# Kernel tuning notes

Hardware: AMD Instinct MI355X
Metric: run time of the kernel (lower is better)

Reference implementation:

```python
import jax, jax.numpy as jnp
import numpy as np

B, N, PS = 8, 2048, 32
P = N // PS          # 64 patches
D, MLP, DEPTH, H, DH = 1024, 2048, 6, 8, 64
INNER = H * DH       # 512
K = 20
EPS = 1e-5


def setup_inputs() -> dict:
    key = jax.random.key(0)
    ks = jax.random.split(key, 16)
    r = lambda i, shape: jax.random.normal(ks[i], shape, dtype=jnp.float32) * 0.02
    return {
        "x": jax.random.normal(ks[0], (B, N, 3), dtype=jnp.float32),
        "x_pos_embed": r(1, (B, P + 1, D)),
        "w1": r(2, (64, 6)),   "g1": jnp.ones(64),  "b1": jnp.zeros(64),
        "w2": r(3, (64, 128)), "g2": jnp.ones(64),  "b2": jnp.zeros(64),
        "w3": r(4, (128, 128)),"g3": jnp.ones(128), "b3": jnp.zeros(128),
        "w4": r(5, (256, 256)),"g4": jnp.ones(256), "b4": jnp.zeros(256),
        "w5": r(6, (D, 512)),  "g5": jnp.ones(D),   "b5": jnp.zeros(D),
        "cls_token": r(7, (1, 1, D)),
        "ln1_g": jnp.ones((DEPTH, D)), "ln1_b": jnp.zeros((DEPTH, D)),
        "wqkv": r(8, (DEPTH, D, 3 * INNER)),
        "wout": r(9, (DEPTH, INNER, D)), "bout": jnp.zeros((DEPTH, D)),
        "ln2_g": jnp.ones((DEPTH, D)), "ln2_b": jnp.zeros((DEPTH, D)),
        "wff1": r(10, (DEPTH, D, MLP)), "bff1": jnp.zeros((DEPTH, MLP)),
        "wff2": r(11, (DEPTH, MLP, D)), "bff2": jnp.zeros((DEPTH, D)),
    }


def _knn(x, k):  # x: [B, C, N] -> neighbor idx [B, N, k]
    xx = jnp.sum(x * x, axis=1)                        # [B, N]
    inner = jnp.einsum('bcn,bcm->bnm', x, x)           # [B, N, N]
    dist = 2.0 * inner - xx[:, :, None] - xx[:, None, :]  # = -||xi-xj||^2
    return jax.lax.top_k(dist, k)[1]


def _graph_feature(x, k):  # x: [B, C, N] -> [B, N, k, 2C]
    idx = _knn(x, k)
    xt = jnp.transpose(x, (0, 2, 1))                   # [B, N, C]
    nbr = jax.vmap(lambda f, i: f[i])(xt, idx)         # gather: [B, N, k, C]
    ctr = jnp.broadcast_to(xt[:, :, None, :], nbr.shape)
    return jnp.concatenate([nbr - ctr, ctr], axis=-1)


def _leaky(v):
    return jnp.where(v >= 0, v, 0.2 * v)


def _edge_conv(x, w, g, b, k):  # EdgeConv block: graph feat -> 1x1 conv -> BN(train) -> lrelu -> max over k
    f = _graph_feature(x, k)                           # [B, N, k, 2C]
    y = jnp.einsum('bnkc,oc->bonk', f, w)              # [B, O, N, k]
    mu = jnp.mean(y, axis=(0, 2, 3), keepdims=True)
    var = jnp.var(y, axis=(0, 2, 3), keepdims=True)
    y = (y - mu) * jax.lax.rsqrt(var + EPS) * g[None, :, None, None] + b[None, :, None, None]
    return jnp.max(_leaky(y), axis=-1)                 # [B, O, N]


def _ln(x, g, b):
    mu = jnp.mean(x, axis=-1, keepdims=True)
    var = jnp.var(x, axis=-1, keepdims=True)
    return (x - mu) * jax.lax.rsqrt(var + EPS) * g + b


def reference(x, x_pos_embed, w1, g1, b1, w2, g2, b2, w3, g3, b3, w4, g4, b4,
              w5, g5, b5, cls_token, ln1_g, ln1_b, wqkv, wout, bout,
              ln2_g, ln2_b, wff1, bff1, wff2, bff2):
    scale = DH ** -0.5
    pts = jnp.transpose(x, (0, 2, 1))                  # [B, 3, N]
    x1 = _edge_conv(pts, w1, g1, b1, K)                # [B, 64, N]
    x2 = _edge_conv(x1, w2, g2, b2, K)                 # [B, 64, N]
    x3 = _edge_conv(x2, w3, g3, b3, K)                 # [B, 128, N]
    x4 = _edge_conv(x3, w4, g4, b4, K)                 # [B, 256, N]
    h = jnp.concatenate([x1, x2, x3, x4], axis=1)      # [B, 512, N]
    y = jnp.einsum('bcn,oc->bon', h, w5)               # conv5 1x1 -> [B, D, N]
    mu = jnp.mean(y, axis=(0, 2), keepdims=True)
    var = jnp.var(y, axis=(0, 2), keepdims=True)
    y = _leaky((y - mu) * jax.lax.rsqrt(var + EPS) * g5[None, :, None] + b5[None, :, None])
    # patch max-pool: 'b (p n) c -> (b p) n c' then max over n
    t = jnp.transpose(y, (0, 2, 1)).reshape(B * P, PS, D)
    t = jnp.max(t, axis=1).reshape(B, P, D)
    t = jnp.concatenate([jnp.broadcast_to(cls_token, (B, 1, D)), t], axis=1)  # [B, P+1, D]
    for i in range(DEPTH):
        t = t + x_pos_embed
        hn = _ln(t, ln1_g[i], ln1_b[i])
        qkv = (hn @ wqkv[i]).reshape(B, P + 1, 3, H, DH)
        q, k_, v = [jnp.transpose(qkv[:, :, j], (0, 2, 1, 3)) for j in range(3)]
        attn = jax.nn.softmax(jnp.einsum('bhld,bhmd->bhlm', q, k_) * scale, axis=-1)
        z = jnp.einsum('bhlm,bhmd->bhld', attn, v)
        z = jnp.transpose(z, (0, 2, 1, 3)).reshape(B, P + 1, INNER)
        t = t + z @ wout[i] + bout[i]
        hn = _ln(t, ln2_g[i], ln2_b[i])
        t = t + jax.nn.gelu(hn @ wff1[i] + bff1[i], approximate=False) @ wff2[i] + bff2[i]
    return t[:, 1:]                                    # [B, P, D]
```

## Files before the change

kernel.cpp:

```cpp
#include <hip/hip_runtime.h>
#include <math.h>

#define BB 8
#define NN 2048
#define PSZ 32
#define PP 64
#define DD 1024
#define MLPD 2048
#define DEPTH_ 6
#define HH 8
#define DHH 64
#define INNER_ 512
#define KK 20
#define TOK 65
#define EPSF 1e-5f

#define GEMM_ACC 1
#define GEMM_GELU 2
#define GEMM_OUTBF16 4

typedef __bf16 bf16_t;
typedef __attribute__((ext_vector_type(8))) __bf16 bf16x8;
typedef __attribute__((ext_vector_type(4))) float f32x4;

__device__ __forceinline__ void async_copy16(const bf16_t* gsrc, bf16_t* ldst) {
    __builtin_amdgcn_global_load_lds(
        (const __attribute__((address_space(1))) unsigned int*)gsrc,
        (__attribute__((address_space(3))) unsigned int*)ldst,
        16, 0, 0);
}

__global__ void transpose_x_kernel(const float* __restrict__ x, float* __restrict__ pts) {
    int gid = blockIdx.x * blockDim.x + threadIdx.x;
    if (gid >= BB * NN * 3) return;
    int c = gid % 3; int n = (gid / 3) % NN; int b = gid / (3 * NN);
    pts[(b * 3 + c) * NN + n] = x[gid];
}

__global__ void sqnorm_kernel(const float* __restrict__ x, int bs, int C, float* __restrict__ xx) {
    int gid = blockIdx.x * blockDim.x + threadIdx.x;
    if (gid >= BB * NN) return;
    int n = gid % NN; int b = gid / NN;
    const float* xp = x + b * bs + n;
    float s = 0.f;
    for (int c = 0; c < C; ++c) { float v = xp[c * NN]; s += v * v; }
    xx[gid] = s;
}

__global__ __launch_bounds__(256) void dist_kernel(const float* __restrict__ x, int bs, int C,
                                                   const float* __restrict__ xx, int b0,
                                                   float* __restrict__ dist) {
    __shared__ __align__(16) float smem[4224];
    float (*As)[132] = (float(*)[132])smem;
    float (*Bs)[132] = (float(*)[132])(smem + 16 * 132);
    float (*tb)[132] = (float(*)[132])smem;

    int q = blockIdx.x;
    int bi = 0, rem = q;
    while (rem >= (16 - bi)) { rem -= (16 - bi); ++bi; }
    int bj = bi + rem;

    int b = b0 + blockIdx.z;
    int n0 = bi * 128, m0 = bj * 128;
    int tid = threadIdx.x;
    int ty = tid >> 4, tx = tid & 15;
    float acc[2][2][4][4] = {};
    const float* xb = x + (long)b * bs;
    for (int k0 = 0; k0 < C; k0 += 16) {
        #pragma unroll
        for (int p = 0; p < 2; ++p) {
            int li = tid + p * 256;
            int i4 = li & 31;
            int kk = li >> 5;
            int c = k0 + kk;
            float4 va = make_float4(0.f, 0.f, 0.f, 0.f);
            float4 vb = va;
            if (c < C) {
                va = *(const float4*)&xb[(long)c * NN + n0 + i4 * 4];
                vb = *(const float4*)&xb[(long)c * NN + m0 + i4 * 4];
            }
            *(float4*)&As[kk][i4 * 4] = va;
            *(float4*)&Bs[kk][i4 * 4] = vb;
        }
        __syncthreads();
        #pragma unroll
        for (int kk = 0; kk < 16; ++kk) {
            float a[2][4], bv[2][4];
            *(float4*)a[0] = *(const float4*)&As[kk][ty * 4];
            *(float4*)a[1] = *(const float4*)&As[kk][64 + ty * 4];
            *(float4*)bv[0] = *(const float4*)&Bs[kk][tx * 4];
            *(float4*)bv[1] = *(const float4*)&Bs[kk][64 + tx * 4];
            #pragma unroll
            for (int ri = 0; ri < 2; ++ri)
                #pragma unroll
                for (int ci = 0; ci < 2; ++ci)
                    #pragma unroll
                    for (int i = 0; i < 4; ++i)
                        #pragma unroll
                        for (int j = 0; j < 4; ++j)
                            acc[ri][ci][i][j] += a[ri][i] * bv[ci][j];
        }
        __syncthreads();
    }
    float* db = dist + (long)blockIdx.z * NN * NN;
    const float* xxb = xx + b * NN;
    float xm[2][4];
    #pragma unroll
    for (int ci = 0; ci < 2; ++ci)
        #pragma unroll
        for (int j = 0; j < 4; ++j)
            xm[ci][j] = xxb[m0 + ci * 64 + tx * 4 + j];
    #pragma unroll
    for (int ri = 0; ri < 2; ++ri)
        #pragma unroll
        for (int i = 0; i < 4; ++i) {
            float xn = xxb[n0 + ri * 64 + ty * 4 + i];
            #pragma unroll
            for (int ci = 0; ci < 2; ++ci)
                #pragma unroll
                for (int j = 0; j < 4; ++j)
                    acc[ri][ci][i][j] = 2.f * acc[ri][ci][i][j] - xn - xm[ci][j];
        }
    #pragma unroll
    for (int ri = 0; ri < 2; ++ri)
        #pragma unroll
        for (int i = 0; i < 4; ++i) {
            int n = n0 + ri * 64 + ty * 4 + i;
            #pragma unroll
            for (int ci = 0; ci < 2; ++ci)
                *(float4*)&db[(long)n * NN + m0 + ci * 64 + tx * 4] = *(float4*)&acc[ri][ci][i][0];
        }
    if (bi != bj) {
        #pragma unroll
        for (int s = 0; s < 4; ++s) {
            __syncthreads();
            int ci = s >> 1;
            if ((tx >> 3) == (s & 1)) {
                #pragma unroll
                for (int ri = 0; ri < 2; ++ri)
                    #pragma unroll
                    for (int j = 0; j < 4; ++j) {
                        float4 v;
                        v.x = acc[ri][ci][0][j];
                        v.y = acc[ri][ci][1][j];
                        v.z = acc[ri][ci][2][j];
                        v.w = acc[ri][ci][3][j];
                        *(float4*)&tb[(tx & 7) * 4 + j][ri * 64 + ty * 4] = v;
                    }
            }
            __syncthreads();
            int r = tid >> 3;
            int c0 = (tid & 7) * 16;
            long orow = (long)(m0 + s * 32 + r) * NN + n0 + c0;
            #pragma unroll
            for (int c4 = 0; c4 < 4; ++c4)
                *(float4*)&db[orow + c4 * 4] = *(const float4*)&tb[r][c0 + c4 * 4];
        }
    }
}

__global__ __launch_bounds__(256) void topk_kernel(const float* __restrict__ dist, int b0,
                                                   int* __restrict__ idx) {
    __shared__ float cval[4][64];
    __shared__ int   cidx[4][64];
    int b = b0 + blockIdx.y;
    int wid = threadIdx.x >> 6, lane = threadIdx.x & 63;
    int n = blockIdx.x * 4 + wid;
    const float* row = dist + ((long)blockIdx.y * NN + n) * NN;
    float vals[32];
    #pragma unroll
    for (int s = 0; s < 32; ++s) vals[s] = row[s * 64 + lane];
    int* op = idx + ((long)b * NN + n) * KK;

    float lm = vals[0];
    #pragma unroll
    for (int s = 1; s < 32; ++s) lm = fmaxf(lm, vals[s]);

    float sv = lm;
    #pragma unroll
    for (int k = 2; k <= 64; k <<= 1) {
        #pragma unroll
        for (int j = k >> 1; j > 0; j >>= 1) {
            float pv = __shfl_xor(sv, j);
            bool lower = (lane & j) == 0;
            bool up = (lane & k) != 0;
            bool ownBetter = sv > pv;
            bool keepOwn = ownBetter ^ (lower == up);
            sv = keepOwn ? sv : pv;
        }
    }
    float t = __shfl(sv, 19);

    int base = 0;
    #pragma unroll
    for (int s = 0; s < 32; ++s) {
        bool q = vals[s] >= t;
        unsigned long long m = __ballot(q);
        int my = base + (int)__builtin_amdgcn_mbcnt_hi((unsigned)(m >> 32),
                         __builtin_amdgcn_mbcnt_lo((unsigned)m, 0u));
        if (q && my < 64) { cval[wid][my] = vals[s]; cidx[wid][my] = s * 64 + lane; }
        base += (int)__popcll(m);
    }
    __asm__ volatile("s_waitcnt lgkmcnt(0)" ::: "memory");

    if (base <= 64) {
        float v = (lane < base) ? cval[wid][lane] : -INFINITY;
        int   ii = (lane < base) ? cidx[wid][lane] : 0x7FFFFFFF;
        #pragma unroll
        for (int k = 2; k <= 64; k <<= 1) {
            #pragma unroll
            for (int j = k >> 1; j > 0; j >>= 1) {
                float pv = __shfl_xor(v, j);
                int   pi = __shfl_xor(ii, j);
                bool lower = (lane & j) == 0;
                bool up = (lane & k) != 0;
                bool ownBetter = (v > pv) || (v == pv && ii < pi);
                bool keepOwn = ownBetter ^ (lower == up);
                if (!keepOwn) { v = pv; ii = pi; }
            }
        }
        if (lane < KK) op[lane] = ii;
    } else {
        for (int kk = 0; kk < KK; ++kk) {
            float bv = vals[0]; int bsl = 0;
            #pragma unroll
            for (int s = 1; s < 32; ++s) if (vals[s] > bv) { bv = vals[s]; bsl = s; }
            int bm = bsl * 64 + lane;
            for (int off = 32; off; off >>= 1) {
                float ov = __shfl_xor(bv, off);
                int om = __shfl_xor(bm, off);
                if (ov > bv || (ov == bv && om < bm)) { bv = ov; bm = om; }
            }
            int wslot = bm >> 6, wlane = bm & 63;
            #pragma unroll
            for (int s = 0; s < 32; ++s)
                if (s == wslot) vals[s] = (lane == wlane) ? -INFINITY : vals[s];
            if (lane == 0) op[kk] = bm;
        }
    }
}

__global__ __launch_bounds__(256) void pq_kernel(const float* __restrict__ x, int bs, int C,
                                                 const float* __restrict__ w, int O,
                                                 float* __restrict__ p, float* __restrict__ q) {
    __shared__ float wT[256][33];
    __shared__ float xs[128][32];
    int b = blockIdx.z;
    int o0 = blockIdx.y * 32;
    int n0 = blockIdx.x * 32;
    int tid = threadIdx.x;
    for (int i = tid; i < 2 * C * 32; i += 256) {
        int c2 = i % (2 * C), o = i / (2 * C);
        wT[c2][o] = w[(o0 + o) * 2 * C + c2];
    }
    for (int i = tid; i < C * 32; i += 256) {
        int nl = i % 32, c = i / 32;
        xs[c][nl] = x[b * bs + c * NN + n0 + nl];
    }
    __syncthreads();
    int o_l = tid & 31;
    int n_base = (tid >> 5) * 4;
    float ps[4] = {0.f, 0.f, 0.f, 0.f};
    float qs[4] = {0.f, 0.f, 0.f, 0.f};
    for (int c = 0; c < C; ++c) {
        float4 xv = *(const float4*)&xs[c][n_base];
        float wa = wT[c][o_l];
        float wb = wT[C + c][o_l];
        float d = wb - wa;
        ps[0] += xv.x * wa; qs[0] += xv.x * d;
        ps[1] += xv.y * wa; qs[1] += xv.y * d;
        ps[2] += xv.z * wa; qs[2] += xv.z * d;
        ps[3] += xv.w * wa; qs[3] += xv.w * d;
    }
    for (int j = 0; j < 4; ++j) {
        long r = (long)(b * NN + n0 + n_base + j) * O + o0 + o_l;
        p[r] = ps[j];
        q[r] = qs[j];
    }
}

__global__ void zero_stats_kernel(double* __restrict__ s1, double* __restrict__ s2) {
    int t = blockIdx.x * blockDim.x + threadIdx.x;
    if (t < 1024) { s1[t] = 0.0; s2[t] = 0.0; }
}

__global__ __launch_bounds__(256) void edge_stats_kernel(const float* __restrict__ p, const float* __restrict__ q,
                                                         const int* __restrict__ idx, int O,
                                                         double* __restrict__ gsum, double* __restrict__ gsumsq) {
    int tid = threadIdx.x;
    int o = tid % O;
    int grp = tid / O;
    int ngrp = 256 / O;
    int rows_per_blk = (BB * NN) / gridDim.x;
    int r0 = blockIdx.x * rows_per_blk;
    double s = 0.0, ss = 0.0;
    for (int r = r0 + grp; r < r0 + rows_per_blk; r += ngrp) {
        int b = r / NN;
        float qv = q[r * O + o];
        for (int k = 0; k < KK; ++k) {
            int j = idx[r * KK + k];
            float v = p[(b * NN + j) * O + o] + qv;
            s += v; ss += (double)v * v;
        }
    }
    atomicAdd(&gsum[o], s);
    atomicAdd(&gsumsq[o], ss);
}

__global__ void bn_finalize_kernel(const double* __restrict__ gsum, const double* __restrict__ gsumsq,
                                   const float* __restrict__ g, const float* __restrict__ bb, int O, double cnt,
                                   float* __restrict__ scale, float* __restrict__ shift) {
    int o = blockIdx.x * blockDim.x + threadIdx.x;
    if (o >= O) return;
    double mean = gsum[o] / cnt;
    double var = gsumsq[o] / cnt - mean * mean;
    float inv = rsqrtf((float)var + EPSF);
    float sc = g[o] * inv;
    scale[o] = sc;
    shift[o] = bb[o] - (float)mean * sc;
}

__global__ void edge_out_kernel(const float* __restrict__ p, const float* __restrict__ q,
                                const int* __restrict__ idx, int O,
                                const float* __restrict__ scale, const float* __restrict__ shift,
                                float* __restrict__ out, int obs) {
    int gid = blockIdx.x * blockDim.x + threadIdx.x;
    if (gid >= BB * NN * O) return;
    int o = gid % O; int n = (gid / O) % NN; int b = gid / (O * NN);
    int r = b * NN + n;
    float qv = q[r * O + o];
    float sc = scale[o], sh = shift[o];
    float m = -INFINITY;
    for (int k = 0; k < KK; ++k) {
        int j = idx[r * KK + k];
        float v = (p[(b * NN + j) * O + o] + qv) * sc + sh;
        v = (v >= 0.f) ? v : 0.2f * v;
        m = fmaxf(m, v);
    }
    out[b * obs + o * NN + n] = m;
}

__global__ __launch_bounds__(256) void transpose_cvt_kernel(const float* __restrict__ in,
                                                            bf16_t* __restrict__ outp,
                                                            int R, int C, long s_in, long s_out) {
    __shared__ float tile[32][33];
    const float* ib = in + (long)blockIdx.z * s_in;
    bf16_t* ob = outp + (long)blockIdx.z * s_out;
    int r0 = blockIdx.y * 32, c0 = blockIdx.x * 32;
    int tx = threadIdx.x & 31, tg = threadIdx.x >> 5;
    for (int i = 0; i < 4; ++i) {
        int r = tg + i * 8;
        tile[r][tx] = ib[(long)(r0 + r) * C + c0 + tx];
    }
    __syncthreads();
    for (int i = 0; i < 4; ++i) {
        int c = tg + i * 8;
        ob[(long)(c0 + c) * R + r0 + tx] = (bf16_t)tile[tx][c];
    }
}

__global__ void cvt_bf16_kernel(const float* __restrict__ in, bf16_t* __restrict__ outp, long n8) {
    long g = (long)blockIdx.x * blockDim.x + threadIdx.x;
    if (g >= n8) return;
    const float4* pp = (const float4*)(in + g * 8);
    float4 a = pp[0], b = pp[1];
    bf16x8 v;
    v[0] = (bf16_t)a.x; v[1] = (bf16_t)a.y; v[2] = (bf16_t)a.z; v[3] = (bf16_t)a.w;
    v[4] = (bf16_t)b.x; v[5] = (bf16_t)b.y; v[6] = (bf16_t)b.z; v[7] = (bf16_t)b.w;
    *(bf16x8*)(outp + g * 8) = v;
}

__global__ __launch_bounds__(256) void gemm_bf16_kernel(const bf16_t* __restrict__ A,
                                                        const bf16_t* __restrict__ Bt,
                                                        const float* __restrict__ bias,
                                                        float* __restrict__ out,
                                                        int M, int Kd, int Nd,
                                                        long sA, long sBt, long sO, int flags) {
    __shared__ __align__(16) bf16_t As[64 * 32];
    __shared__ __align__(16) bf16_t Bs[64 * 32];
    const bf16_t* Ab = A + (long)blockIdx.z * sA;
    const bf16_t* Bb = Bt + (long)blockIdx.z * sBt;
    int row0 = blockIdx.y * 64, col0 = blockIdx.x * 64;
    int tid = threadIdx.x;
    int lane = tid & 63, wv = tid >> 6;
    int wm = wv >> 1, wn = wv & 1;
    int srow = tid & 63;
    int sk = wv * 8;
    const bf16_t* ap = Ab + (long)(row0 + srow) * Kd + sk;
    const bf16_t* bp = Bb + (long)(col0 + srow) * Kd + sk;
    bf16_t* lA = &As[wv * 512];
    bf16_t* lB = &Bs[wv * 512];
    f32x4 acc[2][2] = {};
    for (int k0 = 0; k0 < Kd; k0 += 32) {
        async_copy16(ap + k0, lA);
        async_copy16(bp + k0, lB);
        __syncthreads();
        int q = lane >> 4, cl = lane & 15;
        bf16x8 a0v = *(const bf16x8*)&As[(q * 64 + wm * 32 + cl) * 8];
        bf16x8 a1v = *(const bf16x8*)&As[(q * 64 + wm * 32 + 16 + cl) * 8];
        bf16x8 b0v = *(const bf16x8*)&Bs[(q * 64 + wn * 32 + cl) * 8];
        bf16x8 b1v = *(const bf16x8*)&Bs[(q * 64 + wn * 32 + 16 + cl) * 8];
        acc[0][0] = __builtin_amdgcn_mfma_f32_16x16x32_bf16(a0v, b0v, acc[0][0], 0, 0, 0);
        acc[0][1] = __builtin_amdgcn_mfma_f32_16x16x32_bf16(a0v, b1v, acc[0][1], 0, 0, 0);
        acc[1][0] = __builtin_amdgcn_mfma_f32_16x16x32_bf16(a1v, b0v, acc[1][0], 0, 0, 0);
        acc[1][1] = __builtin_amdgcn_mfma_f32_16x16x32_bf16(a1v, b1v, acc[1][1], 0, 0, 0);
        __syncthreads();
    }
    int q = lane >> 4, cl = lane & 15;
    float* Obf = out + (long)blockIdx.z * sO;
    bf16_t* Obh = (bf16_t*)out + (long)blockIdx.z * sO;
    for (int mt = 0; mt < 2; ++mt)
        for (int nt = 0; nt < 2; ++nt)
            #pragma unroll
            for (int r = 0; r < 4; ++r) {
                int row = row0 + wm * 32 + mt * 16 + q * 4 + r;
                if (row >= M) continue;
                int col = col0 + wn * 32 + nt * 16 + cl;
                float v = acc[mt][nt][r];
                if (bias) v += bias[col];
                if (flags & GEMM_GELU) v = 0.5f * v * (1.f + erff(v * 0.70710678118654752f));
                long oidx = (long)row * Nd + col;
                if (flags & GEMM_OUTBF16) Obh[oidx] = (bf16_t)v;
                else if (flags & GEMM_ACC) Obf[oidx] += v;
                else Obf[oidx] = v;
            }
}

__global__ __launch_bounds__(256) void bn5_stats_bf16_kernel(const bf16_t* __restrict__ y5,
                                                             const float* __restrict__ g,
                                                             const float* __restrict__ bb,
                                                             float* __restrict__ scale, float* __restrict__ shift) {
    __shared__ double ssum[256], ssq[256];
    int d = blockIdx.x;
    int tid = threadIdx.x;
    double s = 0.0, sq = 0.0;
    for (int b = 0; b < BB; ++b) {
        const bf16_t* row = y5 + ((long)b * DD + d) * NN;
        for (int n = tid; n < NN; n += 256) { float v = (float)row[n]; s += v; sq += (double)v * v; }
    }
    ssum[tid] = s; ssq[tid] = sq;
    __syncthreads();
    for (int st = 128; st > 0; st >>= 1) {
        if (tid < st) { ssum[tid] += ssum[tid + st]; ssq[tid] += ssq[tid + st]; }
        __syncthreads();
    }
    if (tid == 0) {
        double cnt = (double)BB * NN;
        double mean = ssum[0] / cnt;
        double var = ssq[0] / cnt - mean * mean;
        float inv = rsqrtf((float)var + EPSF);
        float sc = g[d] * inv;
        scale[d] = sc;
        shift[d] = bb[d] - (float)mean * sc;
    }
}

__global__ void pool_bf16_kernel(const bf16_t* __restrict__ y5, const float* __restrict__ scale,
                                 const float* __restrict__ shift, const float* __restrict__ cls,
                                 float* __restrict__ t) {
    int gid = blockIdx.x * blockDim.x + threadIdx.x;
    if (gid >= BB * TOK * DD) return;
    int d = gid % DD; int l = (gid / DD) % TOK; int b = gid / (DD * TOK);
    float v;
    if (l == 0) {
        v = cls[d];
    } else {
        int pp = l - 1;
        const bf16_t* row = y5 + ((long)b * DD + d) * NN + pp * PSZ;
        float sc = scale[d], sh = shift[d];
        float m = -INFINITY;
        for (int i = 0; i < PSZ; ++i) {
            float u = (float)row[i] * sc + sh;
            u = (u >= 0.f) ? u : 0.2f * u;
            m = fmaxf(m, u);
        }
        v = m;
    }
    t[gid] = v;
}

__global__ __launch_bounds__(256) void ln_kernel(float* __restrict__ t, const float* __restrict__ pos,
                                                 const float* __restrict__ g, const float* __restrict__ bb,
                                                 bf16_t* __restrict__ hn, int addpos) {
    __shared__ double s1[256], s2[256];
    long r = blockIdx.x;
    int tid = threadIdx.x;
    float vals[4];
    double s = 0.0, sq = 0.0;
    for (int i = 0; i < 4; ++i) {
        int d = tid + i * 256;
        float v = t[r * DD + d];
        if (addpos) { v += pos[r * DD + d]; t[r * DD + d] = v; }
        vals[i] = v; s += v; sq += (double)v * v;
    }
    s1[tid] = s; s2[tid] = sq;
    __syncthreads();
    for (int st = 128; st > 0; st >>= 1) {
        if (tid < st) { s1[tid] += s1[tid + st]; s2[tid] += s2[tid + st]; }
        __syncthreads();
    }
    double mean = s1[0] / DD;
    float var = (float)(s2[0] / DD - mean * mean);
    float fm = (float)mean;
    float inv = rsqrtf(var + EPSF);
    for (int i = 0; i < 4; ++i) {
        int d = tid + i * 256;
        hn[r * DD + d] = (bf16_t)((vals[i] - fm) * inv * g[d] + bb[d]);
    }
}

__global__ __launch_bounds__(256) void attn_kernel(const float* __restrict__ qkv, bf16_t* __restrict__ z) {
    __shared__ float ks[TOK][DHH + 1];
    __shared__ float vs[TOK][DHH + 1];
    __shared__ float ss[TOK][TOK];
    int bh = blockIdx.x;
    int b = bh / HH, h = bh % HH;
    int tid = threadIdx.x;
    for (int i = tid; i < TOK * DHH; i += 256) {
        int l = i / DHH, d = i % DHH;
        long base = (long)(b * TOK + l) * 1536;
        ks[l][d] = qkv[base + 512 + h * DHH + d];
        vs[l][d] = qkv[base + 1024 + h * DHH + d];
    }
    __syncthreads();
    for (int i = tid; i < TOK * TOK; i += 256) {
        int l = i / TOK, m = i % TOK;
        const float* qrow = qkv + (long)(b * TOK + l) * 1536 + h * DHH;
        float acc = 0.f;
        for (int d = 0; d < DHH; ++d) acc += qrow[d] * ks[m][d];
        ss[l][m] = acc * 0.125f;
    }
    __syncthreads();
    if (tid < TOK) {
        float mx = -INFINITY;
        for (int m = 0; m < TOK; ++m) mx = fmaxf(mx, ss[tid][m]);
        float sum = 0.f;
        for (int m = 0; m < TOK; ++m) { float e = expf(ss[tid][m] - mx); ss[tid][m] = e; sum += e; }
        float invs = 1.f / sum;
        for (int m = 0; m < TOK; ++m) ss[tid][m] *= invs;
    }
    __syncthreads();
    for (int i = tid; i < TOK * DHH; i += 256) {
        int l = i / DHH, d = i % DHH;
        float acc = 0.f;
        for (int m = 0; m < TOK; ++m) acc += ss[l][m] * vs[m][d];
        z[(long)(b * TOK + l) * INNER_ + h * DHH + d] = (bf16_t)acc;
    }
}

__global__ void final_kernel(const float* __restrict__ t, float* __restrict__ out) {
    int gid = blockIdx.x * blockDim.x + threadIdx.x;
    if (gid >= BB * PP * DD) return;
    int d = gid % DD; int p = (gid / DD) % PP; int b = gid / (DD * PP);
    out[gid] = t[((long)b * TOK + 1 + p) * DD + d];
}

static inline int ceil_div(long a, long b) { return (int)((a + b - 1) / b); }

extern "C" void kernel_launch(void* const* d_in, const int* in_sizes, int n_in,
                              void* d_out, int out_size, void* d_ws, size_t ws_size,
                              hipStream_t stream) {
    const float* x    = (const float*)d_in[0];
    const float* pos  = (const float*)d_in[1];
    const float* w1   = (const float*)d_in[2];
    const float* g1   = (const float*)d_in[3];
    const float* b1   = (const float*)d_in[4];
    const float* w2   = (const float*)d_in[5];
    const float* g2   = (const float*)d_in[6];
    const float* b2   = (const float*)d_in[7];
    const float* w3   = (const float*)d_in[8];
    const float* g3   = (const float*)d_in[9];
    const float* b3   = (const float*)d_in[10];
    const float* w4   = (const float*)d_in[11];
    const float* g4   = (const float*)d_in[12];
    const float* b4   = (const float*)d_in[13];
    const float* w5   = (const float*)d_in[14];
    const float* g5   = (const float*)d_in[15];
    const float* b5   = (const float*)d_in[16];
    const float* cls  = (const float*)d_in[17];
    const float* ln1g = (const float*)d_in[18];
    const float* ln1b = (const float*)d_in[19];
    const float* wqkv = (const float*)d_in[20];
    const float* wout = (const float*)d_in[21];
    const float* bout = (const float*)d_in[22];
    const float* ln2g = (const float*)d_in[23];
    const float* ln2b = (const float*)d_in[24];
    const float* wff1 = (const float*)d_in[25];
    const float* bff1 = (const float*)d_in[26];
    const float* wff2 = (const float*)d_in[27];
    const float* bff2 = (const float*)d_in[28];
    float* out = (float*)d_out;

    char* ws = (char*)d_ws;
    size_t off = 0;
    auto alloc = [&](size_t bytes) -> char* {
        char* ptr = ws + off;
        off = (off + bytes + 255) & ~(size_t)255;
        return ptr;
    };
    float*  h      = (float*)alloc((size_t)BB * 512 * NN * 4);
    float*  t      = (float*)alloc((size_t)BB * TOK * DD * 4);
    bf16_t* hnb    = (bf16_t*)alloc((size_t)BB * TOK * DD * 4);
    float*  qkvb   = (float*)alloc((size_t)BB * TOK * 1536 * 4);
    bf16_t* zbb    = (bf16_t*)alloc((size_t)BB * TOK * INNER_ * 4);
    bf16_t* ubb    = (bf16_t*)alloc((size_t)BB * TOK * MLPD * 4);
    double* dsum   = (double*)alloc(1024 * 8);
    double* dsq    = (double*)alloc(1024 * 8);
    float*  scaleb = (float*)alloc(1024 * 4);
    float*  shiftb = (float*)alloc(1024 * 4);
    size_t ubase = off;

    size_t uoff = ubase;
    auto ualloc = [&](size_t bytes) -> char* {
        char* ptr = ws + uoff;
        uoff = (uoff + bytes + 255) & ~(size_t)255;
        return ptr;
    };
    float* pts  = (float*)ualloc((size_t)BB * 3 * NN * 4);
    float* xx   = (float*)ualloc((size_t)BB * NN * 4);
    int*   idxb = (int*)  ualloc((size_t)BB * NN * KK * 4);
    float* pbuf = (float*)ualloc((size_t)BB * NN * 256 * 4);
    float* qbuf = (float*)ualloc((size_t)BB * NN * 256 * 4);
    size_t dist_rel = uoff - ubase;
    float* distb = (float*)(ws + uoff);

    size_t voff = ubase;
    auto valloc = [&](size_t bytes) -> char* {
        char* ptr = ws + voff;
        voff = (voff + bytes + 255) & ~(size_t)255;
        return ptr;
    };
    bf16_t* hT     = (bf16_t*)valloc((size_t)BB * NN * 512 * 2);
    bf16_t* wTqkv  = (bf16_t*)valloc((size_t)DEPTH_ * 1536 * DD * 2);
    bf16_t* wTout  = (bf16_t*)valloc((size_t)DEPTH_ * DD * INNER_ * 2);
    bf16_t* wTff1  = (bf16_t*)valloc((size_t)DEPTH_ * MLPD * DD * 2);
    bf16_t* wTff2  = (bf16_t*)valloc((size_t)DEPTH_ * DD * MLPD * 2);
    bf16_t* w5b    = (bf16_t*)valloc((size_t)DD * 512 * 2);
    size_t stage_bf16 = voff - ubase;

    size_t conv_full  = dist_rel + (size_t)BB * NN * NN * 4;
    size_t conv_batch = dist_rel + (size_t)NN * NN * 4;

    auto mx = [](size_t a, size_t b) { return a > b ? a : b; };
    bool use_bf16 = ws_size >= ubase + mx(conv_batch, stage_bf16);
    bool full     = ws_size >= ubase + mx(conv_full, stage_bf16);
    if (!use_bf16) return;
    bf16_t* y5bf = (bf16_t*)h;

    transpose_x_kernel<<<ceil_div((long)BB * NN * 3, 256), 256, 0, stream>>>(x, pts);

    const int NTRI = 136;
    auto run_conv = [&](const float* xin, int xbs, int C, const float* w,
                        const float* g, const float* bb, float* hout, int O) {
        sqnorm_kernel<<<ceil_div((long)BB * NN, 256), 256, 0, stream>>>(xin, xbs, C, xx);
        if (full) {
            dist_kernel<<<dim3(NTRI, 1, BB), 256, 0, stream>>>(xin, xbs, C, xx, 0, distb);
            topk_kernel<<<dim3(NN / 4, BB), 256, 0, stream>>>(distb, 0, idxb);
        } else {
            for (int b = 0; b < BB; ++b) {
                dist_kernel<<<dim3(NTRI, 1, 1), 256, 0, stream>>>(xin, xbs, C, xx, b, distb);
                topk_kernel<<<dim3(NN / 4, 1), 256, 0, stream>>>(distb, b, idxb);
            }
        }
        {
            dim3 grid(NN / 32, O / 32, BB);
            pq_kernel<<<grid, 256, 0, stream>>>(xin, xbs, C, w, O, pbuf, qbuf);
        }
        zero_stats_kernel<<<4, 256, 0, stream>>>(dsum, dsq);
        edge_stats_kernel<<<256, 256, 0, stream>>>(pbuf, qbuf, idxb, O, dsum, dsq);
        bn_finalize_kernel<<<1, 256, 0, stream>>>(dsum, dsq, g, bb, O, (double)BB * NN * KK, scaleb, shiftb);
        edge_out_kernel<<<ceil_div((long)BB * NN * O, 256), 256, 0, stream>>>(
            pbuf, qbuf, idxb, O, scaleb, shiftb, hout, 512 * NN);
    };
    run_conv(pts, 3 * NN, 3, w1, g1, b1, h, 64);
    run_conv(h, 512 * NN, 64, w2, g2, b2, h + 64 * NN, 64);
    run_conv(h + 64 * NN, 512 * NN, 64, w3, g3, b3, h + 128 * NN, 128);
    run_conv(h + 128 * NN, 512 * NN, 128, w4, g4, b4, h + 256 * NN, 256);

    const int M = BB * TOK;

    transpose_cvt_kernel<<<dim3(NN / 32, 512 / 32, BB), 256, 0, stream>>>(
        h, hT, 512, NN, (long)512 * NN, (long)NN * 512);
    transpose_cvt_kernel<<<dim3(1536 / 32, DD / 32, DEPTH_), 256, 0, stream>>>(
        wqkv, wTqkv, DD, 1536, (long)DD * 1536, (long)1536 * DD);
    transpose_cvt_kernel<<<dim3(DD / 32, INNER_ / 32, DEPTH_), 256, 0, stream>>>(
        wout, wTout, INNER_, DD, (long)INNER_ * DD, (long)DD * INNER_);
    transpose_cvt_kernel<<<dim3(MLPD / 32, DD / 32, DEPTH_), 256, 0, stream>>>(
        wff1, wTff1, DD, MLPD, (long)DD * MLPD, (long)MLPD * DD);
    transpose_cvt_kernel<<<dim3(DD / 32, MLPD / 32, DEPTH_), 256, 0, stream>>>(
        wff2, wTff2, MLPD, DD, (long)MLPD * DD, (long)DD * MLPD);
    cvt_bf16_kernel<<<ceil_div((long)DD * 512 / 8, 256), 256, 0, stream>>>(w5, w5b, (long)DD * 512 / 8);

    gemm_bf16_kernel<<<dim3(NN / 64, DD / 64, BB), 256, 0, stream>>>(
        w5b, hT, nullptr, (float*)y5bf, DD, 512, NN, 0L, (long)NN * 512, (long)DD * NN, GEMM_OUTBF16);
    bn5_stats_bf16_kernel<<<DD, 256, 0, stream>>>(y5bf, g5, b5, scaleb, shiftb);
    pool_bf16_kernel<<<ceil_div((long)BB * TOK * DD, 256), 256, 0, stream>>>(y5bf, scaleb, shiftb, cls, t);

    for (int i = 0; i < DEPTH_; ++i) {
        ln_kernel<<<M, 256, 0, stream>>>(t, pos, ln1g + i * DD, ln1b + i * DD, hnb, 1);
        gemm_bf16_kernel<<<dim3(1536 / 64, ceil_div(M, 64), 1), 256, 0, stream>>>(
            hnb, wTqkv + (size_t)i * 1536 * DD, nullptr, qkvb, M, DD, 1536, 0L, 0L, 0L, 0);
        attn_kernel<<<BB * HH, 256, 0, stream>>>(qkvb, zbb);
        gemm_bf16_kernel<<<dim3(DD / 64, ceil_div(M, 64), 1), 256, 0, stream>>>(
            zbb, wTout + (size_t)i * DD * INNER_, bout + i * DD, t, M, INNER_, DD, 0L, 0L, 0L, GEMM_ACC);
        ln_kernel<<<M, 256, 0, stream>>>(t, nullptr, ln2g + i * DD, ln2b + i * DD, hnb, 0);
        gemm_bf16_kernel<<<dim3(MLPD / 64, ceil_div(M, 64), 1), 256, 0, stream>>>(
            hnb, wTff1 + (size_t)i * MLPD * DD, bff1 + i * MLPD, (float*)ubb, M, DD, MLPD,
            0L, 0L, 0L, GEMM_GELU | GEMM_OUTBF16);
        gemm_bf16_kernel<<<dim3(DD / 64, ceil_div(M, 64), 1), 256, 0, stream>>>(
            ubb, wTff2 + (size_t)i * DD * MLPD, bff2 + i * DD, t, M, MLPD, DD, 0L, 0L, 0L, GEMM_ACC);
    }

    final_kernel<<<ceil_div((long)BB * PP * DD, 256), 256, 0, stream>>>(t, out);
}
```

Baseline: 2.018 ms.

## Fuse edge-conv stats and max/min gather, finalize via affine monotonicity

Adds a single gather pass that computes the batch-norm sums and also the per-row max and min of the k neighbour values. A small finalize kernel then applies the BN affine and leaky ReLU to the max (or to the min when the scale is negative) and writes the transposed output through a shared-memory tile. This removes the second pass over the k gathered neighbours in edge_out. In exchange it writes and reads max/min buffers that reuse the distance scratch region. The new path is taken only when the full workspace is available.

```diff
diff --git a/kernel.cpp b/kernel.cpp
--- a/kernel.cpp
+++ b/kernel.cpp
@@ -284,6 +284,75 @@
     if (t < 1024) { s1[t] = 0.0; s2[t] = 0.0; }
 }
 
+__global__ __launch_bounds__(256) void edge_gather_kernel(const float* __restrict__ p,
+                                                          const float* __restrict__ q,
+                                                          const int* __restrict__ idx, int O,
+                                                          double* __restrict__ gsum,
+                                                          double* __restrict__ gsumsq,
+                                                          float* __restrict__ maxb,
+                                                          float* __restrict__ minb) {
+    int tid = threadIdx.x;
+    int o = tid % O;
+    int grp = tid / O;
+    int ngrp = 256 / O;
+    int rows_per_blk = (BB * NN) / gridDim.x;
+    int r0 = blockIdx.x * rows_per_blk;
+    double s = 0.0, ss = 0.0;
+    for (int r = r0 + grp; r < r0 + rows_per_blk; r += ngrp) {
+        int b = r / NN;
+        float qv = q[(long)r * O + o];
+        const int* ip = idx + (long)r * KK;
+        float mx = -INFINITY, mn = INFINITY;
+        for (int k = 0; k < KK; ++k) {
+            int j = ip[k];
+            float v = p[(long)(b * NN + j) * O + o] + qv;
+            s += v; ss += (double)v * v;
+            mx = fmaxf(mx, v); mn = fminf(mn, v);
+        }
+        maxb[(long)r * O + o] = mx;
+        minb[(long)r * O + o] = mn;
+    }
+    atomicAdd(&gsum[o], s);
+    atomicAdd(&gsumsq[o], ss);
+}
+
+__global__ void bn_finalize_kernel(const double* __restrict__ gsum, const double* __restrict__ gsumsq,
+                                   const float* __restrict__ g, const float* __restrict__ bb, int O, double cnt,
+                                   float* __restrict__ scale, float* __restrict__ shift) {
+    int o = blockIdx.x * blockDim.x + threadIdx.x;
+    if (o >= O) return;
+    double mean = gsum[o] / cnt;
+    double var = gsumsq[o] / cnt - mean * mean;
+    float inv = rsqrtf((float)var + EPSF);
+    float sc = g[o] * inv;
+    scale[o] = sc;
+    shift[o] = bb[o] - (float)mean * sc;
+}
+
+__global__ __launch_bounds__(256) void edge_finalize_kernel(const float* __restrict__ maxb,
+                                                            const float* __restrict__ minb, int O,
+                                                            const float* __restrict__ scale,
+                                                            const float* __restrict__ shift,
+                                                            float* __restrict__ out, int obs) {
+    __shared__ float tile[32][33];
+    int b = blockIdx.z;
+    int o0 = blockIdx.y * 32, n0 = blockIdx.x * 32;
+    int tx = threadIdx.x & 31, tg = threadIdx.x >> 5;
+    float sc = scale[o0 + tx], sh = shift[o0 + tx];
+    for (int i = 0; i < 4; ++i) {
+        int n = tg + i * 8;
+        long rr = (long)(b * NN + n0 + n) * O + o0 + tx;
+        float base = (sc >= 0.f) ? maxb[rr] : minb[rr];
+        float a = sc * base + sh;
+        tile[n][tx] = (a >= 0.f) ? a : 0.2f * a;
+    }
+    __syncthreads();
+    for (int i = 0; i < 4; ++i) {
+        int o = tg + i * 8;
+        out[(long)b * obs + (long)(o0 + o) * NN + n0 + tx] = tile[tx][o];
+    }
+}
+
 __global__ __launch_bounds__(256) void edge_stats_kernel(const float* __restrict__ p, const float* __restrict__ q,
                                                          const int* __restrict__ idx, int O,
                                                          double* __restrict__ gsum, double* __restrict__ gsumsq) {
@@ -305,19 +374,6 @@
     }
     atomicAdd(&gsum[o], s);
     atomicAdd(&gsumsq[o], ss);
-}
-
-__global__ void bn_finalize_kernel(const double* __restrict__ gsum, const double* __restrict__ gsumsq,
-                                   const float* __restrict__ g, const float* __restrict__ bb, int O, double cnt,
-                                   float* __restrict__ scale, float* __restrict__ shift) {
-    int o = blockIdx.x * blockDim.x + threadIdx.x;
-    if (o >= O) return;
-    double mean = gsum[o] / cnt;
-    double var = gsumsq[o] / cnt - mean * mean;
-    float inv = rsqrtf((float)var + EPSF);
-    float sc = g[o] * inv;
-    scale[o] = sc;
-    shift[o] = bb[o] - (float)mean * sc;
 }
 
 __global__ void edge_out_kernel(const float* __restrict__ p, const float* __restrict__ q,
@@ -623,6 +679,8 @@
     float* qbuf = (float*)ualloc((size_t)BB * NN * 256 * 4);
     size_t dist_rel = uoff - ubase;
     float* distb = (float*)(ws + uoff);
+    float* maxb  = distb;
+    float* minb  = distb + (size_t)BB * NN * 256;
 
     size_t voff = ubase;
     auto valloc = [&](size_t bytes) -> char* {
@@ -667,10 +725,17 @@
             pq_kernel<<<grid, 256, 0, stream>>>(xin, xbs, C, w, O, pbuf, qbuf);
         }
         zero_stats_kernel<<<4, 256, 0, stream>>>(dsum, dsq);
-        edge_stats_kernel<<<256, 256, 0, stream>>>(pbuf, qbuf, idxb, O, dsum, dsq);
-        bn_finalize_kernel<<<1, 256, 0, stream>>>(dsum, dsq, g, bb, O, (double)BB * NN * KK, scaleb, shiftb);
-        edge_out_kernel<<<ceil_div((long)BB * NN * O, 256), 256, 0, stream>>>(
-            pbuf, qbuf, idxb, O, scaleb, shiftb, hout, 512 * NN);
+        if (full) {
+            edge_gather_kernel<<<256, 256, 0, stream>>>(pbuf, qbuf, idxb, O, dsum, dsq, maxb, minb);
+            bn_finalize_kernel<<<1, 256, 0, stream>>>(dsum, dsq, g, bb, O, (double)BB * NN * KK, scaleb, shiftb);
+            edge_finalize_kernel<<<dim3(NN / 32, O / 32, BB), 256, 0, stream>>>(
+                maxb, minb, O, scaleb, shiftb, hout, 512 * NN);
+        } else {
+            edge_stats_kernel<<<256, 256, 0, stream>>>(pbuf, qbuf, idxb, O, dsum, dsq);
+            bn_finalize_kernel<<<1, 256, 0, stream>>>(dsum, dsq, g, bb, O, (double)BB * NN * KK, scaleb, shiftb);
+            edge_out_kernel<<<ceil_div((long)BB * NN * O, 256), 256, 0, stream>>>(
+                pbuf, qbuf, idxb, O, scaleb, shiftb, hout, 512 * NN);
+        }
     };
     run_conv(pts, 3 * NN, 3, w1, g1, b1, h, 64);
     run_conv(h, 512 * NN, 64, w2, g2, b2, h + 64 * NN, 64);
```

New measurement: 2.122 ms. +5.1%, slower.
